# Kernel tuning notes

Hardware: AMD Instinct MI355X
Metric: run time of the kernel (lower is better)

The kernel has to match this reference:

```python
import jax, jax.numpy as jnp
import numpy as np

B, S, D = 2048, 200, 128   # batch, n_steps, embedding dim per vector
H = 64                      # hidden_dim
MASK_SCALE = 1e10


def setup_inputs() -> dict:
    key = jax.random.key(0)
    ks = jax.random.split(key, 6)
    his = jax.random.normal(ks[0], (B, S, D), dtype=jnp.float32)
    target = jax.random.normal(ks[1], (B, 1, D), dtype=jnp.float32)
    # mask == 1.0 marks padded history positions (they get -1e10 added pre-softmax)
    mask = (jax.random.uniform(ks[2], (B, S)) < 0.3).astype(jnp.float32)
    W = jax.random.normal(ks[3], (3 * D, H), dtype=jnp.float32) * 0.1
    W_bias = jnp.full((H,), 0.1, dtype=jnp.float32)
    O = jax.random.normal(ks[4], (H, 1), dtype=jnp.float32) * 0.1
    O_bias = jnp.full((1,), 0.1, dtype=jnp.float32)
    return {"his": his, "target": target, "mask": mask,
            "W": W, "W_bias": W_bias, "O": O, "O_bias": O_bias}


def reference(his, target, mask, W, W_bias, O, O_bias):
    tgt = jnp.broadcast_to(target, his.shape)          # [B,S,D] tile over steps
    diff = his - tgt
    att_vec = jnp.concatenate([his, diff, tgt], axis=2)  # [B,S,3D]
    h = jax.nn.relu(jnp.einsum('bsf,fh->bsh', att_vec, W) + W_bias)  # [B,S,H]
    alpha = jnp.einsum('bsh,ho->bso', h, O) + O_bias   # [B,S,1]
    alpha = alpha[:, :, 0] - mask * MASK_SCALE         # [B,S]
    attn = jax.nn.softmax(alpha, axis=-1)              # [B,S]
    out = jnp.einsum('bs,bsd->bd', attn, his)          # weighted-sum pooling
    return out
```

## Files before the change

### kernel.cpp

```cpp
#include <hip/hip_runtime.h>

#define B_ 2048
#define S_ 200
#define D_ 128
#define H_ 64
#define KB_ 8
#define GRID_ (B_ / KB_)
#define MASK_SCALE 1e10f

typedef __attribute__((ext_vector_type(8))) short short8_t;
typedef __attribute__((ext_vector_type(4))) float f32x4;
typedef __attribute__((ext_vector_type(4))) unsigned short ushort4_t;

__device__ __forceinline__ unsigned short f2bf(float f) {
    unsigned u = __float_as_uint(f);
    unsigned r = (u + 0x7fffu + ((u >> 16) & 1u)) >> 16;
    return (unsigned short)r;
}
__device__ __forceinline__ float bf2f(unsigned short v) {
    return __uint_as_float(((unsigned)v) << 16);
}
__device__ __forceinline__ unsigned cvt_pk_bf16(float lo, float hi) {
    unsigned r;
    asm("v_cvt_pk_bf16_f32 %0, %1, %2" : "=v"(r) : "v"(lo), "v"(hi));
    return r;
}
__device__ __forceinline__ void bar() {
    asm volatile("s_waitcnt lgkmcnt(0)\n\ts_barrier" ::: "memory");
}

__global__ __launch_bounds__(512, 2) void fused_kernel(const float* __restrict__ his,
                                                       const float* __restrict__ mask,
                                                       const float* __restrict__ target,
                                                       const float* __restrict__ W,
                                                       const float* __restrict__ W_bias,
                                                       const float* __restrict__ Ovec,
                                                       float* __restrict__ out) {
    __shared__ unsigned short hisb[2][S_ * D_];
    __shared__ float alph[208];
    __shared__ float attw[208];
    __shared__ float red8[8];
    __shared__ float red8b[8];
    __shared__ float ov_s[H_];
    __shared__ float tpp[8 * H_];
    __shared__ float pool_s[7 * D_];

    const int t    = threadIdx.x;
    const int lane = t & 63;
    const int wv   = t >> 6;
    const int lm   = lane & 15;
    const int q    = lane >> 4;
    const int b0   = blockIdx.x * KB_;

    if (t < H_) ov_s[t] = Ovec[t];
    const float wb = (wv == 0) ? W_bias[lane] : 0.f;

    short8_t bfrag[16];
    float4 wsl[4];
    float mk;

    {
        const float4* hb4 = (const float4*)(his + (size_t)b0 * S_ * D_);
        float4 x0[13];
        #pragma unroll
        for (int j = 0; j < 13; ++j) {
            int i = t + j * 512;
            if (i < 6400) x0[j] = hb4[i];
        }
        const float4* W4 = (const float4*)W;
        float4 w1v[4], w2v[4], w3v[4];
        #pragma unroll
        for (int k = 0; k < 4; ++k) {
            int j = t + k * 512;
            w1v[k] = W4[j];
            w2v[k] = W4[j + 2048];
            w3v[k] = W4[j + 4096];
        }
        mk = (t < S_) ? mask[(size_t)b0 * S_ + t] : 0.f;
        const float4* tg4 = (const float4*)(target + (size_t)b0 * D_) + wv * 4;
        float4 tg0[4];
        #pragma unroll
        for (int k = 0; k < 4; ++k) tg0[k] = tg4[k];
        __builtin_amdgcn_sched_barrier(0);

        unsigned short* wf_s = hisb[1];
        float* wdt_s = (float*)((char*)hisb[1] + 16384);
        #pragma unroll
        for (int k = 0; k < 4; ++k) {
            int j = t + k * 512;
            int e = 4 * j;
            int d = e >> 6;
            int h = e & 63;
            float whc[4] = { w1v[k].x + w2v[k].x, w1v[k].y + w2v[k].y,
                             w1v[k].z + w2v[k].z, w1v[k].w + w2v[k].w };
            float wdc[4] = { w3v[k].x - w2v[k].x, w3v[k].y - w2v[k].y,
                             w3v[k].z - w2v[k].z, w3v[k].w - w2v[k].w };
            int kt = d >> 5, qd = (d >> 3) & 3, jj = d & 7;
            #pragma unroll
            for (int c = 0; c < 4; ++c) {
                int hh = h + c;
                int nt = hh >> 4, lmh = hh & 15;
                int ln = (qd << 4) | lmh;
                wf_s[((kt * 4 + nt) * 64 + ln) * 8 + jj] = f2bf(whc[c]);
                wdt_s[hh * D_ + d] = wdc[c];
            }
        }
        __syncthreads();

        #pragma unroll
        for (int f = 0; f < 16; ++f)
            bfrag[f] = *(const short8_t*)(wf_s + (size_t)(f * 64 + lane) * 8);
        #pragma unroll
        for (int k = 0; k < 4; ++k)
            wsl[k] = *(const float4*)(wdt_s + lane * D_ + wv * 16 + k * 4);

        {
            float acc = wb;
            #pragma unroll
            for (int k = 0; k < 4; ++k) {
                acc = fmaf(tg0[k].x, wsl[k].x, acc);
                acc = fmaf(tg0[k].y, wsl[k].y, acc);
                acc = fmaf(tg0[k].z, wsl[k].z, acc);
                acc = fmaf(tg0[k].w, wsl[k].w, acc);
            }
            tpp[wv * 64 + lane] = acc;
        }
        __syncthreads();

        #pragma unroll
        for (int j = 0; j < 13; ++j) {
            int i = t + j * 512;
            if (i < 6400) {
                int s = i >> 5, d8 = i & 31;
                int pc = (d8 >> 1) ^ (s & 15);
                uint2 v;
                v.x = cvt_pk_bf16(x0[j].x, x0[j].y);
                v.y = cvt_pk_bf16(x0[j].z, x0[j].w);
                *(uint2*)((char*)hisb[0] + s * 256 + pc * 16 + (d8 & 1) * 8) = v;
            }
        }
    }
    __syncthreads();

    int cur = 0;
    for (int n = 0; n < KB_; ++n) {
        const int b = b0 + n;
        const bool more = (n + 1 < KB_);
        const unsigned short* hb = hisb[cur];

        float th[4];
        #pragma unroll
        for (int nt = 0; nt < 4; ++nt) {
            int h = nt * 16 + lm;
            float s0 = tpp[h] + tpp[64 + h] + tpp[128 + h] + tpp[192 + h];
            float s1 = tpp[256 + h] + tpp[320 + h] + tpp[384 + h] + tpp[448 + h];
            th[nt] = s0 + s1;
        }

        float4 x[13];
        float4 tg[4];
        float mkn = 0.f;
        if (more) {
            const float4* hb4n = (const float4*)(his + (size_t)(b + 1) * S_ * D_);
            #pragma unroll
            for (int j = 0; j < 13; ++j) {
                int i = t + j * 512;
                if (i < 6400) x[j] = hb4n[i];
            }
            const float4* tg4 = (const float4*)(target + (size_t)(b + 1) * D_) + wv * 4;
            #pragma unroll
            for (int k = 0; k < 4; ++k) tg[k] = tg4[k];
            if (t < S_) mkn = mask[(size_t)(b + 1) * S_ + t];
        }
        __builtin_amdgcn_sched_barrier(0);

        #pragma unroll
        for (int tt = 0; tt < 2; ++tt) {
            int tile = wv + tt * 8;
            if (tile < 13) {
                int row0 = tile * 16;
                int ar = row0 + lm; if (ar > S_ - 1) ar = S_ - 1;

                f32x4 acc[4];
                #pragma unroll
                for (int nt = 0; nt < 4; ++nt) acc[nt] = (f32x4){0.f, 0.f, 0.f, 0.f};
                #pragma unroll
                for (int kt = 0; kt < 4; ++kt) {
                    int c = (kt * 4 + q) ^ (ar & 15);
                    short8_t av = *(const short8_t*)((const char*)hb + ar * 256 + c * 16);
                    #pragma unroll
                    for (int nt = 0; nt < 4; ++nt)
                        acc[nt] = __builtin_amdgcn_mfma_f32_16x16x32_bf16(av, bfrag[kt * 4 + nt], acc[nt], 0, 0, 0);
                }
                float part[4];
                #pragma unroll
                for (int r = 0; r < 4; ++r) {
                    float sum = 0.f;
                    #pragma unroll
                    for (int nt = 0; nt < 4; ++nt) {
                        int h = nt * 16 + lm;
                        float v = acc[nt][r] + th[nt];
                        v = fmaxf(v, 0.f);
                        sum = fmaf(v, ov_s[h], sum);
                    }
                    part[r] = sum;
                }
                #pragma unroll
                for (int off = 1; off < 16; off <<= 1) {
                    #pragma unroll
                    for (int r = 0; r < 4; ++r)
                        part[r] += __shfl_xor(part[r], off);
                }
                if (lm == 0) {
                    #pragma unroll
                    for (int r = 0; r < 4; ++r)
                        alph[row0 + q * 4 + r] = part[r];
                }
            }
        }
        bar();

        float a = (t < S_) ? alph[t] - mk * MASK_SCALE : -INFINITY;
        float m = a;
        #pragma unroll
        for (int off = 1; off < 64; off <<= 1) m = fmaxf(m, __shfl_xor(m, off));
        if (lane == 0) red8[wv] = m;
        bar();
        m = red8[0];
        #pragma unroll
        for (int k = 1; k < 8; ++k) m = fmaxf(m, red8[k]);
        float e = (t < S_) ? __expf(a - m) : 0.f;
        if (t < S_) attw[t] = e;
        float ssum = e;
        #pragma unroll
        for (int off = 1; off < 64; off <<= 1) ssum += __shfl_xor(ssum, off);
        if (lane == 0) red8b[wv] = ssum;
        bar();
        float tot = red8b[0];
        #pragma unroll
        for (int k = 1; k < 8; ++k) tot += red8b[k];
        const float inv = 1.f / tot;

        const int d8 = t & 31;
        const int sg = t >> 5;
        float acc0 = 0.f, acc1 = 0.f, acc2 = 0.f, acc3 = 0.f;
        #pragma unroll 4
        for (int s = sg; s < S_; s += 16) {
            float w = attw[s];
            int pc = (d8 >> 1) ^ (s & 15);
            ushort4_t v = *(const ushort4_t*)((const char*)hb + s * 256 + pc * 16 + (d8 & 1) * 8);
            acc0 = fmaf(w, bf2f(v[0]), acc0);
            acc1 = fmaf(w, bf2f(v[1]), acc1);
            acc2 = fmaf(w, bf2f(v[2]), acc2);
            acc3 = fmaf(w, bf2f(v[3]), acc3);
        }
        acc0 += __shfl_xor(acc0, 32);
        acc1 += __shfl_xor(acc1, 32);
        acc2 += __shfl_xor(acc2, 32);
        acc3 += __shfl_xor(acc3, 32);
        if (wv && lane < 32) {
            float4 p; p.x = acc0; p.y = acc1; p.z = acc2; p.w = acc3;
            *(float4*)(&pool_s[(wv - 1) * D_ + d8 * 4]) = p;
        }

        if (more) {
            unsigned short* hn = hisb[cur ^ 1];
            #pragma unroll
            for (int j = 0; j < 13; ++j) {
                int i = t + j * 512;
                if (i < 6400) {
                    int s = i >> 5, d8c = i & 31;
                    int pc = (d8c >> 1) ^ (s & 15);
                    uint2 v;
                    v.x = cvt_pk_bf16(x[j].x, x[j].y);
                    v.y = cvt_pk_bf16(x[j].z, x[j].w);
                    *(uint2*)((char*)hn + s * 256 + pc * 16 + (d8c & 1) * 8) = v;
                }
            }
            float acc = wb;
            #pragma unroll
            for (int k = 0; k < 4; ++k) {
                acc = fmaf(tg[k].x, wsl[k].x, acc);
                acc = fmaf(tg[k].y, wsl[k].y, acc);
                acc = fmaf(tg[k].z, wsl[k].z, acc);
                acc = fmaf(tg[k].w, wsl[k].w, acc);
            }
            tpp[wv * 64 + lane] = acc;
        }
        bar();

        if (wv == 0 && lane < 32) {
            #pragma unroll
            for (int k = 0; k < 7; ++k) {
                const float4 p = *(const float4*)(&pool_s[k * D_ + d8 * 4]);
                acc0 += p.x; acc1 += p.y; acc2 += p.z; acc3 += p.w;
            }
            float4 o;
            o.x = acc0 * inv; o.y = acc1 * inv; o.z = acc2 * inv; o.w = acc3 * inv;
            *(float4*)(out + (size_t)b * D_ + d8 * 4) = o;
        }

        mk = mkn;
        cur ^= 1;
    }
}

extern "C" void kernel_launch(void* const* d_in, const int* in_sizes, int n_in,
                              void* d_out, int out_size, void* d_ws, size_t ws_size,
                              hipStream_t stream) {
    const float* his    = (const float*)d_in[0];
    const float* target = (const float*)d_in[1];
    const float* mask   = (const float*)d_in[2];
    const float* W      = (const float*)d_in[3];
    const float* W_bias = (const float*)d_in[4];
    const float* Ovec   = (const float*)d_in[5];
    float* out = (float*)d_out;

    fused_kernel<<<GRID_, 512, 0, stream>>>(his, mask, target, W, W_bias, Ovec, out);
}
```

Baseline: 302.7 us.

## Deepen his prefetch pipeline to two batches ahead with double-buffered tpp

Global loads of his, target and mask for batch n+2 are now issued at the end of iteration n, right after the registers holding batch n+1 have been packed to LDS. Before, each batch's data was loaded at the start of the previous iteration. The prologue loads batches b0 and b0+1 up front, and the target projection buffer tpp is double-buffered so the next batch's partial sums can be written without a race. The aim is to give the global loads a full iteration of latency to hide behind compute. The cost is keeping 13 float4 registers live across the whole MFMA/softmax phase, which may raise register pressure at 2 blocks per CU.

```diff
diff --git a/kernel.cpp b/kernel.cpp
--- a/kernel.cpp
+++ b/kernel.cpp
@@ -42,7 +42,7 @@
     __shared__ float red8[8];
     __shared__ float red8b[8];
     __shared__ float ov_s[H_];
-    __shared__ float tpp[8 * H_];
+    __shared__ float tpp[2][8 * H_];
     __shared__ float pool_s[7 * D_];
 
     const int t    = threadIdx.x;
@@ -57,16 +57,11 @@
 
     short8_t bfrag[16];
     float4 wsl[4];
-    float mk;
+    float4 x[13];
+    float4 tg[4];
+    float mk, mkn;
 
     {
-        const float4* hb4 = (const float4*)(his + (size_t)b0 * S_ * D_);
-        float4 x0[13];
-        #pragma unroll
-        for (int j = 0; j < 13; ++j) {
-            int i = t + j * 512;
-            if (i < 6400) x0[j] = hb4[i];
-        }
         const float4* W4 = (const float4*)W;
         float4 w1v[4], w2v[4], w3v[4];
         #pragma unroll
@@ -76,11 +71,34 @@
             w2v[k] = W4[j + 2048];
             w3v[k] = W4[j + 4096];
         }
+        const float4* hb4 = (const float4*)(his + (size_t)b0 * S_ * D_);
+        float4 x0[13];
+        #pragma unroll
+        for (int j = 0; j < 13; ++j) {
+            int i = t + j * 512;
+            if (i < 6400) x0[j] = hb4[i];
+        }
+        float4 tg0[4];
+        {
+            const float4* tg4 = (const float4*)(target + (size_t)b0 * D_) + wv * 4;
+            #pragma unroll
+            for (int k = 0; k < 4; ++k) tg0[k] = tg4[k];
+        }
         mk = (t < S_) ? mask[(size_t)b0 * S_ + t] : 0.f;
-        const float4* tg4 = (const float4*)(target + (size_t)b0 * D_) + wv * 4;
-        float4 tg0[4];
-        #pragma unroll
-        for (int k = 0; k < 4; ++k) tg0[k] = tg4[k];
+        {
+            const float4* tg4 = (const float4*)(target + (size_t)(b0 + 1) * D_) + wv * 4;
+            #pragma unroll
+            for (int k = 0; k < 4; ++k) tg[k] = tg4[k];
+        }
+        mkn = (t < S_) ? mask[(size_t)(b0 + 1) * S_ + t] : 0.f;
+        {
+            const float4* hb4n = (const float4*)(his + (size_t)(b0 + 1) * S_ * D_);
+            #pragma unroll
+            for (int j = 0; j < 13; ++j) {
+                int i = t + j * 512;
+                if (i < 6400) x[j] = hb4n[i];
+            }
+        }
         __builtin_amdgcn_sched_barrier(0);
 
         unsigned short* wf_s = hisb[1];
@@ -105,7 +123,7 @@
                 wdt_s[hh * D_ + d] = wdc[c];
             }
         }
-        __syncthreads();
+        bar();
 
         #pragma unroll
         for (int f = 0; f < 16; ++f)
@@ -123,9 +141,9 @@
                 acc = fmaf(tg0[k].z, wsl[k].z, acc);
                 acc = fmaf(tg0[k].w, wsl[k].w, acc);
             }
-            tpp[wv * 64 + lane] = acc;
-        }
-        __syncthreads();
+            tpp[0][wv * 64 + lane] = acc;
+        }
+        bar();
 
         #pragma unroll
         for (int j = 0; j < 13; ++j) {
@@ -139,40 +157,24 @@
                 *(uint2*)((char*)hisb[0] + s * 256 + pc * 16 + (d8 & 1) * 8) = v;
             }
         }
+        bar();
     }
-    __syncthreads();
-
-    int cur = 0;
+
     for (int n = 0; n < KB_; ++n) {
         const int b = b0 + n;
-        const bool more = (n + 1 < KB_);
-        const unsigned short* hb = hisb[cur];
-
+        const int p = n & 1;
+        const unsigned short* hb = hisb[p];
+        float mk2 = 0.f;
+
+        const float* tpc = tpp[p];
         float th[4];
         #pragma unroll
         for (int nt = 0; nt < 4; ++nt) {
             int h = nt * 16 + lm;
-            float s0 = tpp[h] + tpp[64 + h] + tpp[128 + h] + tpp[192 + h];
-            float s1 = tpp[256 + h] + tpp[320 + h] + tpp[384 + h] + tpp[448 + h];
+            float s0 = tpc[h] + tpc[64 + h] + tpc[128 + h] + tpc[192 + h];
+            float s1 = tpc[256 + h] + tpc[320 + h] + tpc[384 + h] + tpc[448 + h];
             th[nt] = s0 + s1;
         }
-
-        float4 x[13];
-        float4 tg[4];
-        float mkn = 0.f;
-        if (more) {
-            const float4* hb4n = (const float4*)(his + (size_t)(b + 1) * S_ * D_);
-            #pragma unroll
-            for (int j = 0; j < 13; ++j) {
-                int i = t + j * 512;
-                if (i < 6400) x[j] = hb4n[i];
-            }
-            const float4* tg4 = (const float4*)(target + (size_t)(b + 1) * D_) + wv * 4;
-            #pragma unroll
-            for (int k = 0; k < 4; ++k) tg[k] = tg4[k];
-            if (t < S_) mkn = mask[(size_t)(b + 1) * S_ + t];
-        }
-        __builtin_amdgcn_sched_barrier(0);
 
         #pragma unroll
         for (int tt = 0; tt < 2; ++tt) {
@@ -259,12 +261,24 @@
         acc2 += __shfl_xor(acc2, 32);
         acc3 += __shfl_xor(acc3, 32);
         if (wv && lane < 32) {
-            float4 p; p.x = acc0; p.y = acc1; p.z = acc2; p.w = acc3;
-            *(float4*)(&pool_s[(wv - 1) * D_ + d8 * 4]) = p;
-        }
-
-        if (more) {
-            unsigned short* hn = hisb[cur ^ 1];
+            float4 pr; pr.x = acc0; pr.y = acc1; pr.z = acc2; pr.w = acc3;
+            *(float4*)(&pool_s[(wv - 1) * D_ + d8 * 4]) = pr;
+        }
+
+        if (n < KB_ - 1) {
+            float acc = wb;
+            #pragma unroll
+            for (int k = 0; k < 4; ++k) {
+                acc = fmaf(tg[k].x, wsl[k].x, acc);
+                acc = fmaf(tg[k].y, wsl[k].y, acc);
+                acc = fmaf(tg[k].z, wsl[k].z, acc);
+                acc = fmaf(tg[k].w, wsl[k].w, acc);
+            }
+            tpp[p ^ 1][wv * 64 + lane] = acc;
+        }
+
+        if (n < KB_ - 1) {
+            unsigned short* hn = hisb[p ^ 1];
             #pragma unroll
             for (int j = 0; j < 13; ++j) {
                 int i = t + j * 512;
@@ -277,23 +291,28 @@
                     *(uint2*)((char*)hn + s * 256 + pc * 16 + (d8c & 1) * 8) = v;
                 }
             }
-            float acc = wb;
-            #pragma unroll
-            for (int k = 0; k < 4; ++k) {
-                acc = fmaf(tg[k].x, wsl[k].x, acc);
-                acc = fmaf(tg[k].y, wsl[k].y, acc);
-                acc = fmaf(tg[k].z, wsl[k].z, acc);
-                acc = fmaf(tg[k].w, wsl[k].w, acc);
-            }
-            tpp[wv * 64 + lane] = acc;
-        }
+        }
+
+        if (n < KB_ - 2) {
+            const float4* tg4 = (const float4*)(target + (size_t)(b + 2) * D_) + wv * 4;
+            #pragma unroll
+            for (int k = 0; k < 4; ++k) tg[k] = tg4[k];
+            if (t < S_) mk2 = mask[(size_t)(b + 2) * S_ + t];
+            const float4* hb4n = (const float4*)(his + (size_t)(b + 2) * S_ * D_);
+            #pragma unroll
+            for (int j = 0; j < 13; ++j) {
+                int i = t + j * 512;
+                if (i < 6400) x[j] = hb4n[i];
+            }
+        }
+        __builtin_amdgcn_sched_barrier(0);
         bar();
 
         if (wv == 0 && lane < 32) {
             #pragma unroll
             for (int k = 0; k < 7; ++k) {
-                const float4 p = *(const float4*)(&pool_s[k * D_ + d8 * 4]);
-                acc0 += p.x; acc1 += p.y; acc2 += p.z; acc3 += p.w;
+                const float4 pr = *(const float4*)(&pool_s[k * D_ + d8 * 4]);
+                acc0 += pr.x; acc1 += pr.y; acc2 += pr.z; acc3 += pr.w;
             }
             float4 o;
             o.x = acc0 * inv; o.y = acc1 * inv; o.z = acc2 * inv; o.w = acc3 * inv;
@@ -301,7 +320,7 @@
         }
 
         mk = mkn;
-        cur ^= 1;
+        mkn = mk2;
     }
 }
 
```

Measured after the change: 303.0 us. No clear change (+0.1%).
